# Performance work log

Hardware: AMD Instinct MI355X
Metric: run time of the kernel (lower is better)

## Reference

```python
import jax, jax.numpy as jnp
import numpy as np

N, E, D, B, C = 50000, 800000, 128, 20000, 40
EPS_BN = 1e-3    # keras BatchNormalization default epsilon
EPS_NRM = 1e-12  # keras ops.nn.normalize epsilon
FFN_DIMS = {"pre": (D, D), "c1p": (D, D), "c1u": (2 * D, D), "c2p": (D, D), "c2u": (2 * D, D), "post": (D, D)}


def setup_inputs() -> dict:
    key = jax.random.key(0)
    ks = jax.random.split(key, 8)
    inp = {
        "node_features": jax.random.normal(ks[0], (N, D), jnp.float32),
        "edges": jax.random.randint(ks[1], (2, E), 0, N, dtype=jnp.int32),
        "edge_w": jax.random.uniform(ks[2], (E,), jnp.float32),
        "input_node_idx": jax.random.randint(ks[3], (B,), 0, N, dtype=jnp.int32),
    }
    for i, (name, (din, dout)) in enumerate(FFN_DIMS.items()):
        kw = jax.random.fold_in(key, 100 + i)
        inp[name + "_g"] = jnp.ones((din,), jnp.float32)
        inp[name + "_be"] = jnp.zeros((din,), jnp.float32)
        inp[name + "_mu"] = jnp.zeros((din,), jnp.float32)
        inp[name + "_var"] = jnp.ones((din,), jnp.float32)
        inp[name + "_w"] = jax.random.normal(kw, (din, dout), jnp.float32) * (1.0 / float(np.sqrt(din)))
        inp[name + "_bi"] = jnp.zeros((dout,), jnp.float32)
    inp["logits_w"] = jax.random.normal(ks[4], (D, C), jnp.float32) * (1.0 / float(np.sqrt(D)))
    inp["logits_b"] = jnp.zeros((C,), jnp.float32)
    return inp


def ffn(x, g, be, mu, var, w, bi):
    # BatchNorm (inference running stats) -> Dropout (identity) -> Dense + exact gelu
    xn = (x - mu) * jax.lax.rsqrt(var + EPS_BN) * g + be
    return jax.nn.gelu(xn @ w + bi, approximate=False)


def l2norm(x):
    n = jnp.sqrt(jnp.sum(x * x, axis=-1, keepdims=True))
    return x / jnp.maximum(n, EPS_NRM)


def graph_conv(x, node_idx, nbr_idx, ew, prep, upd):
    # gather neighbours -> prepare FFN -> edge-weighted -> segment_sum (reduce='sum')
    msgs = ffn(x[nbr_idx], *prep) * ew[:, None]                         # [E, D]
    red = jax.ops.segment_sum(msgs, node_idx, num_segments=x.shape[0])  # [N, D]
    h = jnp.concatenate([x, red], axis=1)                               # [N, 2D] (combination='concat')
    return l2norm(ffn(h, *upd))                                         # normalize=True


def reference(node_features, edges, edge_w, input_node_idx,
              pre_g, pre_be, pre_mu, pre_var, pre_w, pre_bi,
              c1p_g, c1p_be, c1p_mu, c1p_var, c1p_w, c1p_bi,
              c1u_g, c1u_be, c1u_mu, c1u_var, c1u_w, c1u_bi,
              c2p_g, c2p_be, c2p_mu, c2p_var, c2p_w, c2p_bi,
              c2u_g, c2u_be, c2u_mu, c2u_var, c2u_w, c2u_bi,
              post_g, post_be, post_mu, post_var, post_w, post_bi,
              logits_w, logits_b):
    ew = edge_w / jnp.sum(edge_w)                       # edge_W normalized at init
    node_idx, nbr_idx = edges[0], edges[1]
    x = ffn(node_features, pre_g, pre_be, pre_mu, pre_var, pre_w, pre_bi)
    x = graph_conv(x, node_idx, nbr_idx, ew,
                   (c1p_g, c1p_be, c1p_mu, c1p_var, c1p_w, c1p_bi),
                   (c1u_g, c1u_be, c1u_mu, c1u_var, c1u_w, c1u_bi)) + x
    x = graph_conv(x, node_idx, nbr_idx, ew,
                   (c2p_g, c2p_be, c2p_mu, c2p_var, c2p_w, c2p_bi),
                   (c2u_g, c2u_be, c2u_mu, c2u_var, c2u_w, c2u_bi)) + x
    x = ffn(x, post_g, post_be, post_mu, post_var, post_w, post_bi)
    return x[input_node_idx] @ logits_w + logits_b      # [B, C]
```

## Files before the change

### kernel.cpp

```cpp
#include <hip/hip_runtime.h>
#include <hip/hip_fp16.h>
#include <math.h>

static constexpr int D = 128;
static constexpr int CAP = 64;
static constexpr float EPS_BN = 1e-3f;

typedef short short8 __attribute__((ext_vector_type(8)));
typedef short short4v __attribute__((ext_vector_type(4)));
typedef float float4v __attribute__((ext_vector_type(4)));

__device__ __forceinline__ float gelu_exact(float x) {
    return 0.5f * x * (1.0f + erff(x * 0.70710678118654752f));
}

__device__ __forceinline__ void f32_to_hilo(float f, short& h, short& l) {
    unsigned u = __float_as_uint(f);
    h = (short)(u >> 16);
    float hf = __uint_as_float(u & 0xFFFF0000u);
    unsigned lu = __float_as_uint(f - hf);
    l = (short)(lu >> 16);
}

__device__ __forceinline__ short f32_to_bf16_rne(float f) {
    unsigned u = __float_as_uint(f);
    u += 0x7FFFu + ((u >> 16) & 1u);
    return (short)(u >> 16);
}

__device__ __forceinline__ void cvt_hilo8(const float4& x, const float4& y, short8& h8, short8& l8) {
    short h, l;
    f32_to_hilo(x.x, h, l); h8[0] = h; l8[0] = l;
    f32_to_hilo(x.y, h, l); h8[1] = h; l8[1] = l;
    f32_to_hilo(x.z, h, l); h8[2] = h; l8[2] = l;
    f32_to_hilo(x.w, h, l); h8[3] = h; l8[3] = l;
    f32_to_hilo(y.x, h, l); h8[4] = h; l8[4] = l;
    f32_to_hilo(y.y, h, l); h8[5] = h; l8[5] = l;
    f32_to_hilo(y.z, h, l); h8[6] = h; l8[6] = l;
    f32_to_hilo(y.w, h, l); h8[7] = h; l8[7] = l;
}

__device__ __forceinline__ short8 cvt_rne8(const float4& x, const float4& y) {
    short8 r;
    r[0] = f32_to_bf16_rne(x.x); r[1] = f32_to_bf16_rne(x.y);
    r[2] = f32_to_bf16_rne(x.z); r[3] = f32_to_bf16_rne(x.w);
    r[4] = f32_to_bf16_rne(y.x); r[5] = f32_to_bf16_rne(y.y);
    r[6] = f32_to_bf16_rne(y.z); r[7] = f32_to_bf16_rne(y.w);
    return r;
}

struct FoldArgs {
    const float* g[6]; const float* be[6]; const float* mu[6];
    const float* var[6]; const float* w[6]; const float* bi[6];
    short* wh[6]; short* wl[6]; float* bp[6]; int K[6];
};

__global__ void k_build(const int* __restrict__ edges, const float* __restrict__ ew,
                        int* __restrict__ cnt, float* __restrict__ sums,
                        unsigned* __restrict__ cw, FoldArgs fa, int E, int N, int fillBlocks) {
    __shared__ float sm[4];
    const int tid = threadIdx.x;
    const int lane = tid & 63, wvi = tid >> 6;

    if ((int)blockIdx.x < fillBlocks) {
        const int g = blockIdx.x & 7;
        const int bid = blockIdx.x >> 3;
        const int gstride = (fillBlocks >> 3) * 256;
        const int N8 = (N + 7) >> 3;
        const int lo = g * N8;
        const int hi = min(lo + N8, N);
        float s = 0.f;
        for (int e = bid * 256 + tid; e < E; e += gstride) {
            int dst = edges[e];
            if (dst >= lo && dst < hi) {
                int src = edges[E + e];
                float w = ew[e];
                s += w;
                unsigned short wb = __half_as_ushort(__float2half(w));
                int idx = atomicAdd(&cnt[dst], 1);
                if (idx < CAP)
                    cw[(size_t)dst * CAP + idx] = ((unsigned)src << 16) | (unsigned)wb;
            }
        }
        for (int off = 32; off > 0; off >>= 1) s += __shfl_down(s, off, 64);
        if (lane == 0) sm[wvi] = s;
        __syncthreads();
        if (tid == 0) {
            float t = sm[0] + sm[1] + sm[2] + sm[3];
            if (t != 0.f) atomicAdd(sums, t);
        }
    } else {
        const int idx = blockIdx.x - fillBlocks;
        const int f = idx >> 7;
        const int c = idx & 127;
        const int K = fa.K[f];
        const float* g = fa.g[f]; const float* be = fa.be[f];
        const float* mu = fa.mu[f]; const float* var = fa.var[f];
        const float* w = fa.w[f]; const float* bi = fa.bi[f];
        short* wh = fa.wh[f]; short* wl = fa.wl[f]; float* bp = fa.bp[f];
        float part = 0.f;
        for (int k = tid; k < K; k += blockDim.x) {
            float a = g[k] / sqrtf(var[k] + EPS_BN);
            float wv = w[k * D + c];
            float prod = a * wv;
            short hh, ll;
            f32_to_hilo(prod, hh, ll);
            wh[c * K + k] = hh;
            wl[c * K + k] = ll;
            part += (be[k] - mu[k] * a) * wv;
        }
        for (int off = 32; off > 0; off >>= 1) part += __shfl_down(part, off, 64);
        if (lane == 0) sm[wvi] = part;
        __syncthreads();
        if (tid == 0) bp[c] = bi[c] + sm[0] + sm[1] + sm[2] + sm[3];
    }
}

__device__ __forceinline__ void accum8(float* acc, const float4& raw, float w) {
    const __half2* hp = (const __half2*)&raw;
    #pragma unroll
    for (int t = 0; t < 4; t++) {
        float2 f = __half22float2(hp[t]);
        acc[t * 2]     += w * f.x;
        acc[t * 2 + 1] += w * f.y;
    }
}

__global__ void k_reduce(const int* __restrict__ cnt, const unsigned* __restrict__ cw,
                         const float* __restrict__ sums, const __half* __restrict__ y,
                         float* __restrict__ red, int N) {
    int n = blockIdx.x * (blockDim.x >> 6) + (threadIdx.x >> 6);
    if (n >= N) return;
    float inv = 1.0f / sums[0];
    int lane = threadIdx.x & 63;
    int sub = lane >> 4;
    int q = lane & 15;
    int count = min(cnt[n], CAP);
    int start = n * CAP;
    int end = start + count;
    float acc[8] = {0.f, 0.f, 0.f, 0.f, 0.f, 0.f, 0.f, 0.f};
    int i = start + sub;
    for (; i + 12 < end; i += 16) {
        unsigned c0 = cw[i];
        unsigned c1 = cw[i + 4];
        unsigned c2 = cw[i + 8];
        unsigned c3 = cw[i + 12];
        float4 r0 = *((const float4*)(y + (size_t)(c0 >> 16) * D) + q);
        float4 r1 = *((const float4*)(y + (size_t)(c1 >> 16) * D) + q);
        float4 r2 = *((const float4*)(y + (size_t)(c2 >> 16) * D) + q);
        float4 r3 = *((const float4*)(y + (size_t)(c3 >> 16) * D) + q);
        float w0 = __half2float(__ushort_as_half((unsigned short)(c0 & 0xFFFFu))) * inv;
        float w1 = __half2float(__ushort_as_half((unsigned short)(c1 & 0xFFFFu))) * inv;
        float w2 = __half2float(__ushort_as_half((unsigned short)(c2 & 0xFFFFu))) * inv;
        float w3 = __half2float(__ushort_as_half((unsigned short)(c3 & 0xFFFFu))) * inv;
        accum8(acc, r0, w0);
        accum8(acc, r1, w1);
        accum8(acc, r2, w2);
        accum8(acc, r3, w3);
    }
    for (; i < end; i += 4) {
        unsigned c = cw[i];
        float4 r = *((const float4*)(y + (size_t)(c >> 16) * D) + q);
        float w = __half2float(__ushort_as_half((unsigned short)(c & 0xFFFFu))) * inv;
        accum8(acc, r, w);
    }
    #pragma unroll
    for (int t = 0; t < 8; t++) {
        acc[t] += __shfl_xor(acc[t], 16, 64);
        acc[t] += __shfl_xor(acc[t], 32, 64);
    }
    if (sub == 0) {
        float4 o0 = {acc[0], acc[1], acc[2], acc[3]};
        float4 o1 = {acc[4], acc[5], acc[6], acc[7]};
        *((float4*)(red + (size_t)n * D + q * 8)) = o0;
        *((float4*)(red + (size_t)n * D + q * 8 + 4)) = o1;
    }
}

template<int K, bool SPLIT3, bool L2RES, bool OUT16, bool GATHER>
__global__ void __launch_bounds__(512) k_ffn(
    const float* __restrict__ A0, const float* __restrict__ A1,
    const short* __restrict__ Wh, const short* __restrict__ Wl,
    const float* __restrict__ bp, const float* __restrict__ resid,
    float* __restrict__ outf, __half* __restrict__ outh, int N,
    const int* __restrict__ gidx)
{
    constexpr int NB = SPLIT3 ? 2 : 1;
    constexpr int WSZ = 128 * K;
    constexpr int NC = K / 64;
    __shared__ short Wlds[NB * WSZ];
    __shared__ float rsum[2][16][4];

    const int tid = threadIdx.x;

    constexpr int ITER = (NB * WSZ) / (512 * 8);
    #pragma unroll
    for (int it = 0; it < ITER; ++it) {
        int s = it * 4096 + tid * 8;
        int buf = s / WSZ;
        int rem = s - buf * WSZ;
        int c = rem / K;
        int kk = (rem & (K - 1)) ^ ((c & 7) << 3);
        const short* src = (buf ? Wl : Wh) + c * K + kk;
        *(short8*)&Wlds[s] = *(const short8*)src;
    }
    __syncthreads();

    const int lane = tid & 63;
    const int wv = tid >> 6;
    const int ssub = wv >> 2;
    const int wc = wv & 3;
    const int m = lane & 15;
    const int quad = lane >> 4;
    const int nstrips = (N + 15) >> 4;
    const int stride = gridDim.x * 2;
    const int base = blockIdx.x * 2 + ssub;

    auto body = [&](int strip, bool active) {
        int rr = active ? strip * 16 + m : m;
        if (rr >= N) rr = N - 1;
        const int r = GATHER ? gidx[rr] : rr;
        const float* pA0 = A0 + (size_t)r * D;
        const float* pA1 = (K == 256) ? (A1 + (size_t)r * D) : pA0;

        float4 a[2][4];
        {
            const float4* s4 = (const float4*)pA0 + quad * 2;
            a[0][0] = s4[0]; a[0][1] = s4[1]; a[0][2] = s4[8]; a[0][3] = s4[9];
        }
        {
            const float4* s4 = (const float4*)(pA0 + 64) + quad * 2;
            a[1][0] = s4[0]; a[1][1] = s4[1]; a[1][2] = s4[8]; a[1][3] = s4[9];
        }

        float4v acc[2];
        acc[0] = (float4v){0.f, 0.f, 0.f, 0.f};
        acc[1] = (float4v){0.f, 0.f, 0.f, 0.f};

        #pragma unroll
        for (int cc = 0; cc < NC; ++cc) {
            #pragma unroll
            for (int ks = 0; ks < 2; ++ks) {
                const int kk = cc * 64 + ks * 32 + quad * 8;
                short8 ah, al;
                if (SPLIT3) cvt_hilo8(a[cc & 1][ks * 2], a[cc & 1][ks * 2 + 1], ah, al);
                else        ah = cvt_rne8(a[cc & 1][ks * 2], a[cc & 1][ks * 2 + 1]);
                #pragma unroll
                for (int tj = 0; tj < 2; ++tj) {
                    const int c = wc * 32 + tj * 16 + m;
                    const int idx = c * K + (kk ^ ((c & 7) << 3));
                    short8 bh = *(const short8*)&Wlds[idx];
                    if (SPLIT3) {
                        short8 bl = *(const short8*)&Wlds[WSZ + idx];
                        acc[tj] = __builtin_amdgcn_mfma_f32_16x16x32_bf16(al, bh, acc[tj], 0, 0, 0);
                        acc[tj] = __builtin_amdgcn_mfma_f32_16x16x32_bf16(ah, bl, acc[tj], 0, 0, 0);
                    }
                    acc[tj] = __builtin_amdgcn_mfma_f32_16x16x32_bf16(ah, bh, acc[tj], 0, 0, 0);
                }
            }
            if (cc + 2 < NC) {
                const int n2 = cc + 2;
                const float* src = (K == 256 && n2 >= 2) ? pA1 : pA0;
                const int kb = (K == 256) ? ((n2 & 1) * 64) : (n2 * 64);
                const float4* s4 = (const float4*)(src + kb) + quad * 2;
                a[cc & 1][0] = s4[0]; a[cc & 1][1] = s4[1];
                a[cc & 1][2] = s4[8]; a[cc & 1][3] = s4[9];
            }
        }

        #pragma unroll
        for (int tj = 0; tj < 2; ++tj) {
            float bv = bp[wc * 32 + tj * 16 + m];
            #pragma unroll
            for (int r4 = 0; r4 < 4; ++r4)
                acc[tj][r4] = gelu_exact(acc[tj][r4] + bv);
        }

        if (L2RES) {
            float ss[4];
            #pragma unroll
            for (int r4 = 0; r4 < 4; ++r4) {
                float v = acc[0][r4] * acc[0][r4] + acc[1][r4] * acc[1][r4];
                v += __shfl_xor(v, 1, 64);
                v += __shfl_xor(v, 2, 64);
                v += __shfl_xor(v, 4, 64);
                v += __shfl_xor(v, 8, 64);
                ss[r4] = v;
            }
            if (m == 0) {
                #pragma unroll
                for (int r4 = 0; r4 < 4; ++r4) rsum[ssub][quad * 4 + r4][wc] = ss[r4];
            }
            __syncthreads();
            #pragma unroll
            for (int r4 = 0; r4 < 4; ++r4) {
                const int rib = quad * 4 + r4;
                float tot = rsum[ssub][rib][0] + rsum[ssub][rib][1]
                          + rsum[ssub][rib][2] + rsum[ssub][rib][3];
                float inv = 1.0f / fmaxf(sqrtf(tot), 1e-12f);
                int row = strip * 16 + rib;
                if (active && row < N) {
                    #pragma unroll
                    for (int tj = 0; tj < 2; ++tj) {
                        int col = wc * 32 + tj * 16 + m;
                        outf[(size_t)row * D + col] = acc[tj][r4] * inv + resid[(size_t)row * D + col];
                    }
                }
            }
            __syncthreads();
        } else {
            #pragma unroll
            for (int r4 = 0; r4 < 4; ++r4) {
                int row = strip * 16 + quad * 4 + r4;
                if (active && row < N) {
                    #pragma unroll
                    for (int tj = 0; tj < 2; ++tj) {
                        int col = wc * 32 + tj * 16 + m;
                        if (OUT16) outh[(size_t)row * D + col] = __float2half(acc[tj][r4]);
                        else       outf[(size_t)row * D + col] = acc[tj][r4];
                    }
                }
            }
        }
    };

    if (L2RES) {
        int rem = nstrips - blockIdx.x * 2;
        int nit = rem > 0 ? (rem + stride - 1) / stride : 0;
        for (int it = 0; it < nit; ++it) {
            int strip = base + it * stride;
            body(strip, strip < nstrips);
        }
    } else {
        for (int strip = base; strip < nstrips; strip += stride)
            body(strip, true);
    }
}

__global__ void k_logits(const float* __restrict__ x,
                         const float* __restrict__ LW, const float* __restrict__ lb,
                         float* __restrict__ out, int B) {
    int wid = blockIdx.x * 4 + (threadIdx.x >> 6);
    int lane = threadIdx.x & 63;
    if (wid >= B) return;
    if (lane >= 40) return;
    float acc = lb[lane];
    const float4* xr = (const float4*)(x + (size_t)wid * D);
    #pragma unroll 4
    for (int k4 = 0; k4 < 32; k4++) {
        float4 xv = xr[k4];
        acc += xv.x * LW[(4 * k4 + 0) * 40 + lane];
        acc += xv.y * LW[(4 * k4 + 1) * 40 + lane];
        acc += xv.z * LW[(4 * k4 + 2) * 40 + lane];
        acc += xv.w * LW[(4 * k4 + 3) * 40 + lane];
    }
    out[(size_t)wid * 40 + lane] = acc;
}

extern "C" void kernel_launch(void* const* d_in, const int* in_sizes, int n_in,
                              void* d_out, int out_size, void* d_ws, size_t ws_size,
                              hipStream_t stream) {
    const float* node_features = (const float*)d_in[0];
    const int*   edges         = (const int*)d_in[1];
    const float* edge_w        = (const float*)d_in[2];
    const int*   input_idx     = (const int*)d_in[3];
    const int N = in_sizes[0] / D;
    const int E = in_sizes[2];
    const int B = in_sizes[3];

    const float* P[6][6];
    for (int f = 0; f < 6; f++)
        for (int q = 0; q < 6; q++)
            P[f][q] = (const float*)d_in[4 + f * 6 + q];
    const float* logits_w = (const float*)d_in[40];
    const float* logits_b = (const float*)d_in[41];

    float* ws = (float*)d_ws;
    size_t nd = (size_t)N * D;
    float* xA  = ws;
    float* y   = ws + nd;
    float* red = ws + 2 * nd;
    float* p   = ws + 3 * nd;
    __half* yh = (__half*)p; p += nd / 2;
    const int Ks[6] = {128, 128, 256, 128, 256, 128};
    short* Wh[6]; short* Wl[6]; float* Bp[6];
    {
        short* sp = (short*)p;
        for (int f = 0; f < 6; f++) {
            Wh[f] = sp; sp += (size_t)Ks[f] * D;
            Wl[f] = sp; sp += (size_t)Ks[f] * D;
        }
        p = (float*)sp;
    }
    for (int f = 0; f < 6; f++) { Bp[f] = p; p += D; }
    int* cnt    = (int*)p; p += N;
    float* sums = p; p += 2;
    unsigned* cw = (unsigned*)p; p += (size_t)N * CAP;

    FoldArgs fa;
    for (int f = 0; f < 6; f++) {
        fa.g[f] = P[f][0]; fa.be[f] = P[f][1]; fa.mu[f] = P[f][2];
        fa.var[f] = P[f][3]; fa.w[f] = P[f][4]; fa.bi[f] = P[f][5];
        fa.wh[f] = Wh[f]; fa.wl[f] = Wl[f]; fa.bp[f] = Bp[f]; fa.K[f] = Ks[f];
    }

    const int fillBlocks = 2048;
    hipMemsetAsync(cnt, 0, ((size_t)N + 2) * sizeof(int), stream);
    k_build<<<fillBlocks + 768, 256, 0, stream>>>(edges, edge_w, cnt, sums, cw, fa, E, N, fillBlocks);

    const int rb = (N + 3) / 4;
    const int g1 = 256;
    const int g2 = 512;
    const int g3 = 1024;

    k_ffn<128, true,  false, false, false><<<g2, 512, 0, stream>>>(node_features, nullptr, Wh[0], Wl[0], Bp[0], nullptr, xA, nullptr, N, nullptr);
    k_ffn<128, false, false, true,  false><<<g3, 512, 0, stream>>>(xA, nullptr, Wh[1], Wl[1], Bp[1], nullptr, nullptr, yh, N, nullptr);
    k_reduce<<<rb, 256, 0, stream>>>(cnt, cw, sums, yh, red, N);
    k_ffn<256, true,  true,  false, false><<<g1, 512, 0, stream>>>(xA, red, Wh[2], Wl[2], Bp[2], xA, y, nullptr, N, nullptr);
    k_ffn<128, false, false, true,  false><<<g3, 512, 0, stream>>>(y, nullptr, Wh[3], Wl[3], Bp[3], nullptr, nullptr, yh, N, nullptr);
    k_reduce<<<rb, 256, 0, stream>>>(cnt, cw, sums, yh, red, N);
    k_ffn<256, true,  true,  false, false><<<g1, 512, 0, stream>>>(y, red, Wh[4], Wl[4], Bp[4], y, xA, nullptr, N, nullptr);
    k_ffn<128, true,  false, false, true ><<<g2, 512, 0, stream>>>(xA, nullptr, Wh[5], Wl[5], Bp[5], nullptr, red, nullptr, B, input_idx);
    k_logits<<<(B + 3) / 4, 256, 0, stream>>>(red, logits_w, logits_b, (float*)d_out, B);
}
```

Before: 462.1 us.

## Co-schedule edge bucket fill with pre-FFN in one kernel

Splits weight folding into its own kernel, then runs the edge-bucketing fill and the first (pre) FFN in a single launch, with even blocks doing the fill and odd blocks doing the MFMA matmul. The aim is to overlap the atomic-heavy, latency-bound edge scatter with the compute-bound pre FFN instead of running them back to back. The fill now uses 512-thread blocks with 64 blocks per group. The FFN half holds 64KB of LDS per block, which may limit occupancy for the fill blocks too.

```diff
diff --git a/kernel.cpp b/kernel.cpp
--- a/kernel.cpp
+++ b/kernel.cpp
@@ -55,22 +55,61 @@
     short* wh[6]; short* wl[6]; float* bp[6]; int K[6];
 };
 
-__global__ void k_build(const int* __restrict__ edges, const float* __restrict__ ew,
-                        int* __restrict__ cnt, float* __restrict__ sums,
-                        unsigned* __restrict__ cw, FoldArgs fa, int E, int N, int fillBlocks) {
+__global__ void k_fold(FoldArgs fa) {
     __shared__ float sm[4];
     const int tid = threadIdx.x;
     const int lane = tid & 63, wvi = tid >> 6;
-
-    if ((int)blockIdx.x < fillBlocks) {
-        const int g = blockIdx.x & 7;
-        const int bid = blockIdx.x >> 3;
-        const int gstride = (fillBlocks >> 3) * 256;
+    const int f = blockIdx.x >> 7;
+    const int c = blockIdx.x & 127;
+    const int K = fa.K[f];
+    const float* g = fa.g[f]; const float* be = fa.be[f];
+    const float* mu = fa.mu[f]; const float* var = fa.var[f];
+    const float* w = fa.w[f]; const float* bi = fa.bi[f];
+    short* wh = fa.wh[f]; short* wl = fa.wl[f]; float* bp = fa.bp[f];
+    float part = 0.f;
+    for (int k = tid; k < K; k += blockDim.x) {
+        float a = g[k] / sqrtf(var[k] + EPS_BN);
+        float wv = w[k * D + c];
+        float prod = a * wv;
+        short hh, ll;
+        f32_to_hilo(prod, hh, ll);
+        wh[c * K + k] = hh;
+        wl[c * K + k] = ll;
+        part += (be[k] - mu[k] * a) * wv;
+    }
+    for (int off = 32; off > 0; off >>= 1) part += __shfl_down(part, off, 64);
+    if (lane == 0) sm[wvi] = part;
+    __syncthreads();
+    if (tid == 0) bp[c] = bi[c] + sm[0] + sm[1] + sm[2] + sm[3];
+}
+
+__global__ void __launch_bounds__(512) k_fillpre(
+    const int* __restrict__ edges, const float* __restrict__ ew,
+    int* __restrict__ cnt, float* __restrict__ sums, unsigned* __restrict__ cw,
+    int E, int N,
+    const float* __restrict__ A0, const short* __restrict__ Wh,
+    const short* __restrict__ Wl, const float* __restrict__ bp,
+    float* __restrict__ outf)
+{
+    constexpr int K = 128;
+    constexpr int WSZ = 128 * K;
+    __shared__ short Wlds[2 * WSZ];
+    __shared__ float sm[8];
+
+    const int tid = threadIdx.x;
+    const int lane = tid & 63;
+    const int wvi = tid >> 6;
+
+    if ((blockIdx.x & 1) == 0) {
+        const int fid = blockIdx.x >> 1;
+        const int g = fid & 7;
+        const int bid = fid >> 3;
+        const int gstride = 64 * 512;
         const int N8 = (N + 7) >> 3;
         const int lo = g * N8;
         const int hi = min(lo + N8, N);
         float s = 0.f;
-        for (int e = bid * 256 + tid; e < E; e += gstride) {
+        for (int e = bid * 512 + tid; e < E; e += gstride) {
             int dst = edges[e];
             if (dst >= lo && dst < hi) {
                 int src = edges[E + e];
@@ -86,33 +125,94 @@
         if (lane == 0) sm[wvi] = s;
         __syncthreads();
         if (tid == 0) {
-            float t = sm[0] + sm[1] + sm[2] + sm[3];
+            float t = 0.f;
+            #pragma unroll
+            for (int i = 0; i < 8; i++) t += sm[i];
             if (t != 0.f) atomicAdd(sums, t);
         }
-    } else {
-        const int idx = blockIdx.x - fillBlocks;
-        const int f = idx >> 7;
-        const int c = idx & 127;
-        const int K = fa.K[f];
-        const float* g = fa.g[f]; const float* be = fa.be[f];
-        const float* mu = fa.mu[f]; const float* var = fa.var[f];
-        const float* w = fa.w[f]; const float* bi = fa.bi[f];
-        short* wh = fa.wh[f]; short* wl = fa.wl[f]; float* bp = fa.bp[f];
-        float part = 0.f;
-        for (int k = tid; k < K; k += blockDim.x) {
-            float a = g[k] / sqrtf(var[k] + EPS_BN);
-            float wv = w[k * D + c];
-            float prod = a * wv;
-            short hh, ll;
-            f32_to_hilo(prod, hh, ll);
-            wh[c * K + k] = hh;
-            wl[c * K + k] = ll;
-            part += (be[k] - mu[k] * a) * wv;
-        }
-        for (int off = 32; off > 0; off >>= 1) part += __shfl_down(part, off, 64);
-        if (lane == 0) sm[wvi] = part;
-        __syncthreads();
-        if (tid == 0) bp[c] = bi[c] + sm[0] + sm[1] + sm[2] + sm[3];
+        return;
+    }
+
+    const int fbid = blockIdx.x >> 1;
+    constexpr int NBLK = 512;
+
+    #pragma unroll
+    for (int it = 0; it < (2 * WSZ) / (512 * 8); ++it) {
+        int s = it * 4096 + tid * 8;
+        int buf = s / WSZ;
+        int rem = s - buf * WSZ;
+        int c = rem / K;
+        int kk = (rem & (K - 1)) ^ ((c & 7) << 3);
+        const short* src = (buf ? Wl : Wh) + c * K + kk;
+        *(short8*)&Wlds[s] = *(const short8*)src;
+    }
+    __syncthreads();
+
+    const int wv = tid >> 6;
+    const int ssub = wv >> 2;
+    const int wc = wv & 3;
+    const int m = lane & 15;
+    const int quad = lane >> 4;
+    const int nstrips = (N + 15) >> 4;
+    const int stride = NBLK * 2;
+
+    for (int strip = fbid * 2 + ssub; strip < nstrips; strip += stride) {
+        int r = strip * 16 + m;
+        if (r >= N) r = N - 1;
+        const float* pA0 = A0 + (size_t)r * D;
+
+        float4 a[2][4];
+        {
+            const float4* s4 = (const float4*)pA0 + quad * 2;
+            a[0][0] = s4[0]; a[0][1] = s4[1]; a[0][2] = s4[8]; a[0][3] = s4[9];
+        }
+        {
+            const float4* s4 = (const float4*)(pA0 + 64) + quad * 2;
+            a[1][0] = s4[0]; a[1][1] = s4[1]; a[1][2] = s4[8]; a[1][3] = s4[9];
+        }
+
+        float4v acc[2];
+        acc[0] = (float4v){0.f, 0.f, 0.f, 0.f};
+        acc[1] = (float4v){0.f, 0.f, 0.f, 0.f};
+
+        #pragma unroll
+        for (int cc = 0; cc < 2; ++cc) {
+            #pragma unroll
+            for (int ks = 0; ks < 2; ++ks) {
+                const int kk = cc * 64 + ks * 32 + quad * 8;
+                short8 ah, al;
+                cvt_hilo8(a[cc][ks * 2], a[cc][ks * 2 + 1], ah, al);
+                #pragma unroll
+                for (int tj = 0; tj < 2; ++tj) {
+                    const int c = wc * 32 + tj * 16 + m;
+                    const int idx = c * K + (kk ^ ((c & 7) << 3));
+                    short8 bh = *(const short8*)&Wlds[idx];
+                    short8 bl = *(const short8*)&Wlds[WSZ + idx];
+                    acc[tj] = __builtin_amdgcn_mfma_f32_16x16x32_bf16(al, bh, acc[tj], 0, 0, 0);
+                    acc[tj] = __builtin_amdgcn_mfma_f32_16x16x32_bf16(ah, bl, acc[tj], 0, 0, 0);
+                    acc[tj] = __builtin_amdgcn_mfma_f32_16x16x32_bf16(ah, bh, acc[tj], 0, 0, 0);
+                }
+            }
+        }
+
+        #pragma unroll
+        for (int tj = 0; tj < 2; ++tj) {
+            float bv = bp[wc * 32 + tj * 16 + m];
+            #pragma unroll
+            for (int r4 = 0; r4 < 4; ++r4)
+                acc[tj][r4] = gelu_exact(acc[tj][r4] + bv);
+        }
+        #pragma unroll
+        for (int r4 = 0; r4 < 4; ++r4) {
+            int row = strip * 16 + quad * 4 + r4;
+            if (row < N) {
+                #pragma unroll
+                for (int tj = 0; tj < 2; ++tj) {
+                    int col = wc * 32 + tj * 16 + m;
+                    outf[(size_t)row * D + col] = acc[tj][r4];
+                }
+            }
+        }
     }
 }
 
@@ -404,16 +504,16 @@
         fa.wh[f] = Wh[f]; fa.wl[f] = Wl[f]; fa.bp[f] = Bp[f]; fa.K[f] = Ks[f];
     }
 
-    const int fillBlocks = 2048;
     hipMemsetAsync(cnt, 0, ((size_t)N + 2) * sizeof(int), stream);
-    k_build<<<fillBlocks + 768, 256, 0, stream>>>(edges, edge_w, cnt, sums, cw, fa, E, N, fillBlocks);
+    k_fold<<<768, 256, 0, stream>>>(fa);
+    k_fillpre<<<1024, 512, 0, stream>>>(edges, edge_w, cnt, sums, cw, E, N,
+                                        node_features, Wh[0], Wl[0], Bp[0], xA);
 
     const int rb = (N + 3) / 4;
     const int g1 = 256;
     const int g2 = 512;
     const int g3 = 1024;
 
-    k_ffn<128, true,  false, false, false><<<g2, 512, 0, stream>>>(node_features, nullptr, Wh[0], Wl[0], Bp[0], nullptr, xA, nullptr, N, nullptr);
     k_ffn<128, false, false, true,  false><<<g3, 512, 0, stream>>>(xA, nullptr, Wh[1], Wl[1], Bp[1], nullptr, nullptr, yh, N, nullptr);
     k_reduce<<<rb, 256, 0, stream>>>(cnt, cw, sums, yh, red, N);
     k_ffn<256, true,  true,  false, false><<<g1, 512, 0, stream>>>(xA, red, Wh[2], Wl[2], Bp[2], xA, y, nullptr, N, nullptr);
```

Measured after the change: 446.8 us. 3.3% less time.
